# Kernel tuning notes

Hardware: AMD Instinct MI355X
Metric: run time of the kernel (lower is better)

## Reference

```python
import jax, jax.numpy as jnp
import numpy as np

N = 50000      # nodes
E = 800000     # directed edges (avg degree 16)
IN, HID, OUT = 256, 128, 16


def setup_inputs() -> dict:
    key = jax.random.key(0)
    ks = jax.random.split(key, 8)
    x = jax.random.normal(ks[0], (N, IN), dtype=jnp.float32)
    edge_index = jax.random.randint(ks[1], (2, E), 0, N)
    W1 = jax.random.normal(ks[2], (IN, HID), dtype=jnp.float32) * (1.0 / np.sqrt(IN))
    b1 = jnp.zeros((HID,), jnp.float32)
    W2 = jax.random.normal(ks[3], (HID, HID), dtype=jnp.float32) * (1.0 / np.sqrt(HID))
    b2 = jnp.zeros((HID,), jnp.float32)
    Wc = jax.random.normal(ks[4], (HID, OUT), dtype=jnp.float32) * (1.0 / np.sqrt(HID))
    bc = jnp.zeros((OUT,), jnp.float32)
    return {"x": x, "W1": W1, "b1": b1, "W2": W2, "b2": b2,
            "Wc": Wc, "bc": bc, "edge_index": edge_index, "conv_time": 30}


def _gcn_norm(edge_index, n, dtype):
    # add self-loops, compute symmetric GCN normalization D^{-1/2}(A+I)D^{-1/2}
    loops = jnp.arange(n)
    src = jnp.concatenate([edge_index[0], loops])
    dst = jnp.concatenate([edge_index[1], loops])
    deg = jax.ops.segment_sum(jnp.ones_like(dst, dtype=dtype), dst, num_segments=n)
    dinv = jnp.where(deg > 0, jax.lax.rsqrt(deg), jnp.zeros_like(deg))
    norm = dinv[src] * dinv[dst]          # [E+N] edge weights
    return src, dst, norm


def _propagate(h, src, dst, norm, n, hops):
    # hops is a static Python int (conv_time)
    for _ in range(hops):
        h = jax.ops.segment_sum(h[src] * norm[:, None], dst, num_segments=n)
    return h


def reference(x, W1, b1, W2, b2, Wc, bc, edge_index, conv_time):
    n = x.shape[0]
    src, dst, norm = _gcn_norm(edge_index, n, x.dtype)
    # conv1: linear only (conv_time = 0)
    h = jax.nn.relu(x @ W1 + b1)
    # dropout is identity in eval mode
    # conv2: linear + conv_time hops of normalized propagation
    h = _propagate(h @ W2 + b2, src, dst, norm, n, int(conv_time))
    h = jax.nn.relu(h)
    # cls: linear + 1 hop
    h = _propagate(h @ Wc + bc, src, dst, norm, n, 1)
    return h
```

## Files before the change

kernel.cpp:

```cpp
#include <hip/hip_runtime.h>
#include <hip/hip_fp16.h>

#define NNODES 50000
#define NEDGES 800000
#define IN_F   256
#define HID_F  128
#define OUT_F  16
#define HOPS   30

typedef unsigned int u32;

union U32H2 { u32 u; __half2 h; };

__device__ inline float2 upk(u32 v) {
    U32H2 t; t.u = v;
    return __half22float2(t.h);
}
__device__ inline u32 pk2(float a, float b) {
    U32H2 t; t.h = __floats2half2_rn(a, b);
    return t.u;
}


__global__ void k_init_deg(int* __restrict__ deg, int n) {
    int i = blockIdx.x * blockDim.x + threadIdx.x;
    if (i < n) deg[i] = 1;
}

__global__ void k_count(const int* __restrict__ dst, int* __restrict__ deg, int e) {
    int i = blockIdx.x * blockDim.x + threadIdx.x;
    if (i < e) atomicAdd(&deg[dst[i]], 1);
}

__global__ void k_dinv(const int* __restrict__ deg, float* __restrict__ dinv, int n) {
    int i = blockIdx.x * blockDim.x + threadIdx.x;
    if (i < n) dinv[i] = rsqrtf((float)deg[i]);
}

__global__ void k_scan1(const int* __restrict__ deg, int* __restrict__ bsums, int n) {
    __shared__ int sh[256];
    int tid = threadIdx.x;
    int i = blockIdx.x * 256 + tid;
    sh[tid] = (i < n) ? deg[i] : 0;
    __syncthreads();
    for (int ofs = 128; ofs > 0; ofs >>= 1) {
        if (tid < ofs) sh[tid] += sh[tid + ofs];
        __syncthreads();
    }
    if (tid == 0) bsums[blockIdx.x] = sh[0];
}

__global__ void k_scan2(int* __restrict__ bsums, int nb, int* __restrict__ rp, int n) {
    if (threadIdx.x == 0 && blockIdx.x == 0) {
        int run = 0;
        for (int b = 0; b < nb; ++b) { int t = bsums[b]; bsums[b] = run; run += t; }
        rp[n] = run;
    }
}

__global__ void k_scan3(const int* __restrict__ deg, const int* __restrict__ bsums,
                        int* __restrict__ rp, int* __restrict__ cursor, int n) {
    __shared__ int sh[256];
    int tid = threadIdx.x;
    int i = blockIdx.x * 256 + tid;
    int v = (i < n) ? deg[i] : 0;
    sh[tid] = v;
    __syncthreads();
    for (int ofs = 1; ofs < 256; ofs <<= 1) {
        int t = 0;
        if (tid >= ofs) t = sh[tid - ofs];
        __syncthreads();
        sh[tid] += t;
        __syncthreads();
    }
    if (i < n) {
        int excl = sh[tid] - v + bsums[blockIdx.x];
        rp[i] = excl;
        cursor[i] = excl;
    }
}

__global__ void k_scatter(const int* __restrict__ src, const int* __restrict__ dst,
                          const float* __restrict__ dinv, int* __restrict__ cursor,
                          int2* __restrict__ ew, int e, int n) {
    int t = blockIdx.x * blockDim.x + threadIdx.x;
    if (t < e) {
        int s = src[t], d = dst[t];
        int pos = atomicAdd(&cursor[d], 1);
        ew[pos] = make_int2(s, __float_as_int(dinv[s] * dinv[d]));
    } else if (t < e + n) {
        int i = t - e;
        int pos = atomicAdd(&cursor[i], 1);
        float di = dinv[i];
        ew[pos] = make_int2(i, __float_as_int(di * di));
    }
}


template<int K, bool RELU, bool HALF_OUT>
__global__ void k_gemm32(const float* __restrict__ A, const float* __restrict__ W,
                         const float* __restrict__ b, void* __restrict__ C, int M) {
    __shared__ float sa[32][K];
    int tid  = threadIdx.x;
    int row0 = blockIdx.x * 32;
    constexpr int KV = K / 4;

    const float4* A4 = reinterpret_cast<const float4*>(A);
    for (int idx = tid; idx < 32 * KV; idx += 256) {
        int r  = idx / KV;
        int c4 = idx % KV;
        int gr = row0 + r;
        float4 v = (gr < M) ? A4[(size_t)gr * KV + c4]
                            : make_float4(0.f, 0.f, 0.f, 0.f);
        *reinterpret_cast<float4*>(&sa[r][c4 * 4]) = v;
    }
    __syncthreads();

    int tc = tid & 31;
    int tr = tid >> 5;
    float4 acc[4];
#pragma unroll
    for (int j = 0; j < 4; ++j) acc[j] = make_float4(0.f, 0.f, 0.f, 0.f);

    const float4* W4 = reinterpret_cast<const float4*>(W);
    for (int k4 = 0; k4 < KV; ++k4) {
        float4 a[4];
#pragma unroll
        for (int j = 0; j < 4; ++j)
            a[j] = *reinterpret_cast<const float4*>(&sa[tr * 4 + j][k4 * 4]);
        const float* af = reinterpret_cast<const float*>(a);
#pragma unroll
        for (int kk = 0; kk < 4; ++kk) {
            float4 wv = W4[(size_t)(k4 * 4 + kk) * 32 + tc];
#pragma unroll
            for (int j = 0; j < 4; ++j) {
                float av = af[j * 4 + kk];
                acc[j].x += av * wv.x; acc[j].y += av * wv.y;
                acc[j].z += av * wv.z; acc[j].w += av * wv.w;
            }
        }
    }

    float4 bb = reinterpret_cast<const float4*>(b)[tc];
#pragma unroll
    for (int j = 0; j < 4; ++j) {
        int r = row0 + tr * 4 + j;
        if (r < M) {
            float4 v;
            v.x = acc[j].x + bb.x; v.y = acc[j].y + bb.y;
            v.z = acc[j].z + bb.z; v.w = acc[j].w + bb.w;
            if (RELU) {
                v.x = fmaxf(v.x, 0.f); v.y = fmaxf(v.y, 0.f);
                v.z = fmaxf(v.z, 0.f); v.w = fmaxf(v.w, 0.f);
            }
            if (HALF_OUT) {
                u32 lo = pk2(v.x, v.y), hi = pk2(v.z, v.w);
                reinterpret_cast<uint2*>(C)[(size_t)r * 32 + tc] = make_uint2(lo, hi);
            } else {
                reinterpret_cast<float4*>(C)[(size_t)r * 32 + tc] = v;
            }
        }
    }
}


template<bool RELU>
__global__ void k_proph(const u32* __restrict__ Hin, u32* __restrict__ Hout,
                        const int* __restrict__ rp, const int2* __restrict__ ew,
                        int n) {
    int grp  = threadIdx.x >> 3;
    int lane = threadIdx.x & 7;
    int node = blockIdx.x * 32 + grp;
    if (node >= n) return;
    int beg = rp[node], end = rp[node + 1];
    const uint4* H4 = reinterpret_cast<const uint4*>(Hin);

    float acc[16];
#pragma unroll
    for (int i = 0; i < 16; ++i) acc[i] = 0.f;

    auto body = [&](int e) {
        int2 p   = ew[e];
        float ww = __int_as_float(p.y);
        size_t base = (size_t)p.x * 16 + lane * 2;
        uint4 v0 = H4[base];
        uint4 v1 = H4[base + 1];
        const u32* vv = reinterpret_cast<const u32*>(&v0);
#pragma unroll
        for (int q = 0; q < 4; ++q) {
            float2 f = upk(vv[q]);
            acc[q * 2 + 0] += ww * f.x;
            acc[q * 2 + 1] += ww * f.y;
        }
        const u32* vw = reinterpret_cast<const u32*>(&v1);
#pragma unroll
        for (int q = 0; q < 4; ++q) {
            float2 f = upk(vw[q]);
            acc[8 + q * 2 + 0] += ww * f.x;
            acc[8 + q * 2 + 1] += ww * f.y;
        }
    };

    int e = beg;
    for (; e + 1 < end; e += 2) { body(e); body(e + 1); }
    if (e < end) body(e);

    if (RELU) {
#pragma unroll
        for (int i = 0; i < 16; ++i) acc[i] = fmaxf(acc[i], 0.f);
    }
    uint4 o0, o1;
    u32* ov = reinterpret_cast<u32*>(&o0);
#pragma unroll
    for (int q = 0; q < 4; ++q) ov[q] = pk2(acc[q * 2], acc[q * 2 + 1]);
    u32* ow = reinterpret_cast<u32*>(&o1);
#pragma unroll
    for (int q = 0; q < 4; ++q) ow[q] = pk2(acc[8 + q * 2], acc[8 + q * 2 + 1]);
    size_t obase = (size_t)node * 16 + lane * 2;
    reinterpret_cast<uint4*>(Hout)[obase]     = o0;
    reinterpret_cast<uint4*>(Hout)[obase + 1] = o1;
}


__global__ void k_cls_h(const u32* __restrict__ Ah, const float* __restrict__ Wc,
                        const float* __restrict__ bc, float* __restrict__ G, int M) {
    __shared__ float sa[64][132];
    __shared__ float4 sw4[512];
    int tid  = threadIdx.x;
    int row0 = blockIdx.x * 64;

    for (int idx = tid; idx < 512; idx += 256)
        sw4[idx] = reinterpret_cast<const float4*>(Wc)[idx];

    const uint4* A4 = reinterpret_cast<const uint4*>(Ah);
    for (int idx = tid; idx < 64 * 16; idx += 256) {
        int r = idx >> 4, c = idx & 15;
        int gr = row0 + r;
        uint4 v = (gr < M) ? A4[(size_t)gr * 16 + c]
                           : make_uint4(0u, 0u, 0u, 0u);
        float* dst = &sa[r][c * 8];
        const u32* vv = reinterpret_cast<const u32*>(&v);
#pragma unroll
        for (int q = 0; q < 4; ++q) {
            float2 f = upk(vv[q]);
            dst[q * 2 + 0] = f.x;
            dst[q * 2 + 1] = f.y;
        }
    }
    __syncthreads();

    int tc = tid & 3;
    int tr = tid >> 2;
    float4 acc = make_float4(0.f, 0.f, 0.f, 0.f);
    for (int k4 = 0; k4 < 32; ++k4) {
        float4 a = *reinterpret_cast<const float4*>(&sa[tr][k4 * 4]);
        const float* af = reinterpret_cast<const float*>(&a);
#pragma unroll
        for (int kk = 0; kk < 4; ++kk) {
            float4 wv = sw4[(k4 * 4 + kk) * 4 + tc];
            float av = af[kk];
            acc.x += av * wv.x; acc.y += av * wv.y;
            acc.z += av * wv.z; acc.w += av * wv.w;
        }
    }
    int r = row0 + tr;
    if (r < M) {
        float4 bb = reinterpret_cast<const float4*>(bc)[tc];
        acc.x += bb.x; acc.y += bb.y; acc.z += bb.z; acc.w += bb.w;
        reinterpret_cast<float4*>(G)[(size_t)r * 4 + tc] = acc;
    }
}


__global__ void k_prop16(const float* __restrict__ Gin, float* __restrict__ Out,
                         const int* __restrict__ rp, const int2* __restrict__ ew,
                         int n) {
    int g    = blockIdx.x * 64 + (threadIdx.x >> 2);
    int lane = threadIdx.x & 3;
    if (g >= n) return;
    int beg = rp[g], end = rp[g + 1];
    const float4* G4 = reinterpret_cast<const float4*>(Gin);
    float ax = 0.f, ay = 0.f, az = 0.f, aw = 0.f;
    for (int e = beg; e < end; ++e) {
        int2 p   = ew[e];
        float ww = __int_as_float(p.y);
        float4 hv = G4[(size_t)p.x * 4 + lane];
        ax += ww * hv.x; ay += ww * hv.y; az += ww * hv.z; aw += ww * hv.w;
    }
    reinterpret_cast<float4*>(Out)[(size_t)g * 4 + lane] = make_float4(ax, ay, az, aw);
}


extern "C" void kernel_launch(void* const* d_in, const int* in_sizes, int n_in,
                              void* d_out, int out_size, void* d_ws, size_t ws_size,
                              hipStream_t stream) {
    const float* x  = (const float*)d_in[0];
    const float* W1 = (const float*)d_in[1];
    const float* b1 = (const float*)d_in[2];
    const float* W2 = (const float*)d_in[3];
    const float* b2 = (const float*)d_in[4];
    const float* Wc = (const float*)d_in[5];
    const float* bc = (const float*)d_in[6];
    const int*   ei = (const int*)d_in[7];
    const int* srcp = ei;
    const int* dstp = ei + NEDGES;
    float* out = (float*)d_out;

    char* p = (char*)d_ws;
    auto alloc = [&](size_t bytes) -> char* {
        char* r = p;
        p += (bytes + 255) & ~(size_t)255;
        return r;
    };
    int*   deg    = (int*)  alloc(NNODES * 4);
    float* dinv   = (float*)alloc(NNODES * 4);
    int*   rp     = (int*)  alloc((NNODES + 1) * 4);
    int*   cursor = (int*)  alloc(NNODES * 4);
    int*   bsums  = (int*)  alloc(256 * 4);
    int2*  ew     = (int2*) alloc((size_t)(NEDGES + NNODES) * 8);
    float* H0     = (float*)alloc((size_t)NNODES * HID_F * 4);
    u32*   Hh0    = (u32*)  alloc((size_t)NNODES * HID_F * 2);
    u32*   Hh1    = (u32*)  alloc((size_t)NNODES * HID_F * 2);
    float* G      = (float*)alloc((size_t)NNODES * OUT_F * 4);

    const int T = 256;
    auto nb = [](int n, int t) { return (n + t - 1) / t; };

    k_init_deg<<<nb(NNODES, T), T, 0, stream>>>(deg, NNODES);
    k_count<<<nb(NEDGES, T), T, 0, stream>>>(dstp, deg, NEDGES);
    k_dinv<<<nb(NNODES, T), T, 0, stream>>>(deg, dinv, NNODES);
    int NB = nb(NNODES, 256);
    k_scan1<<<NB, 256, 0, stream>>>(deg, bsums, NNODES);
    k_scan2<<<1, 1, 0, stream>>>(bsums, NB, rp, NNODES);
    k_scan3<<<NB, 256, 0, stream>>>(deg, bsums, rp, cursor, NNODES);
    k_scatter<<<nb(NEDGES + NNODES, T), T, 0, stream>>>(srcp, dstp, dinv, cursor,
                                                        ew, NEDGES, NNODES);

    int GB = nb(NNODES, 32);
    k_gemm32<IN_F,  true,  false><<<GB, 256, 0, stream>>>(x,  W1, b1, H0,  NNODES);
    k_gemm32<HID_F, false, true ><<<GB, 256, 0, stream>>>(H0, W2, b2, Hh0, NNODES);

    u32* cur = Hh0;
    u32* nxt = Hh1;
    int PB = nb(NNODES, 32);
    for (int i = 0; i < HOPS; ++i) {
        if (i == HOPS - 1)
            k_proph<true ><<<PB, 256, 0, stream>>>(cur, nxt, rp, ew, NNODES);
        else
            k_proph<false><<<PB, 256, 0, stream>>>(cur, nxt, rp, ew, NNODES);
        u32* t = cur; cur = nxt; nxt = t;
    }

    k_cls_h<<<nb(NNODES, 64), 256, 0, stream>>>(cur, Wc, bc, G, NNODES);
    k_prop16<<<nb(NNODES, 64), 256, 0, stream>>>(G, out, rp, ew, NNODES);
}
```

Before: 1.238 ms.

## Split propagation feature dimension across four blocks per node tile

The propagation kernel now splits each node's 128 half features into four 32-feature chunks, each handled by a separate block. A node gets 4 lanes per chunk, each loading one 16-byte vector per edge. Edge records are read with nontemporal 64-bit loads and outputs are written with nontemporal stores. The aim is more parallelism and lower register pressure. The cost is that every chunk block re-reads the edge list (4x edge-index traffic), and the feature gathers become narrower. An unroll pragma is also added to the GEMM k-loop.

```diff
diff --git a/kernel.cpp b/kernel.cpp
--- a/kernel.cpp
+++ b/kernel.cpp
@@ -9,6 +9,8 @@
 #define HOPS   30
 
 typedef unsigned int u32;
+typedef u32 u32x4 __attribute__((ext_vector_type(4)));
+typedef unsigned long long u64;
 
 union U32H2 { u32 u; __half2 h; };
 
@@ -123,6 +125,7 @@
     for (int j = 0; j < 4; ++j) acc[j] = make_float4(0.f, 0.f, 0.f, 0.f);
 
     const float4* W4 = reinterpret_cast<const float4*>(W);
+#pragma unroll 2
     for (int k4 = 0; k4 < KV; ++k4) {
         float4 a[4];
 #pragma unroll
@@ -165,39 +168,34 @@
 
 
 template<bool RELU>
-__global__ void k_proph(const u32* __restrict__ Hin, u32* __restrict__ Hout,
-                        const int* __restrict__ rp, const int2* __restrict__ ew,
-                        int n) {
-    int grp  = threadIdx.x >> 3;
-    int lane = threadIdx.x & 7;
-    int node = blockIdx.x * 32 + grp;
+__global__ void k_proph4(const u32* __restrict__ Hin, u32* __restrict__ Hout,
+                         const int* __restrict__ rp, const int2* __restrict__ ew,
+                         int n) {
+    int chunk = blockIdx.x & 3;
+    int tile  = blockIdx.x >> 2;
+    int grp   = threadIdx.x >> 2;
+    int lane  = threadIdx.x & 3;
+    int node  = tile * 64 + grp;
     if (node >= n) return;
     int beg = rp[node], end = rp[node + 1];
-    const uint4* H4 = reinterpret_cast<const uint4*>(Hin);
-
-    float acc[16];
-#pragma unroll
-    for (int i = 0; i < 16; ++i) acc[i] = 0.f;
+    const u32x4* H4 = reinterpret_cast<const u32x4*>(Hin);
+    const u64* ew8  = reinterpret_cast<const u64*>(ew);
+    int off = chunk * 4 + lane;
+
+    float acc[8];
+#pragma unroll
+    for (int i = 0; i < 8; ++i) acc[i] = 0.f;
 
     auto body = [&](int e) {
-        int2 p   = ew[e];
-        float ww = __int_as_float(p.y);
-        size_t base = (size_t)p.x * 16 + lane * 2;
-        uint4 v0 = H4[base];
-        uint4 v1 = H4[base + 1];
-        const u32* vv = reinterpret_cast<const u32*>(&v0);
+        u64 pw   = __builtin_nontemporal_load(ew8 + e);
+        int s    = (int)(u32)pw;
+        float ww = __int_as_float((u32)(pw >> 32));
+        u32x4 v  = H4[(size_t)s * 16 + off];
 #pragma unroll
         for (int q = 0; q < 4; ++q) {
-            float2 f = upk(vv[q]);
+            float2 f = upk(v[q]);
             acc[q * 2 + 0] += ww * f.x;
             acc[q * 2 + 1] += ww * f.y;
-        }
-        const u32* vw = reinterpret_cast<const u32*>(&v1);
-#pragma unroll
-        for (int q = 0; q < 4; ++q) {
-            float2 f = upk(vw[q]);
-            acc[8 + q * 2 + 0] += ww * f.x;
-            acc[8 + q * 2 + 1] += ww * f.y;
         }
     };
 
@@ -207,18 +205,13 @@
 
     if (RELU) {
 #pragma unroll
-        for (int i = 0; i < 16; ++i) acc[i] = fmaxf(acc[i], 0.f);
-    }
-    uint4 o0, o1;
-    u32* ov = reinterpret_cast<u32*>(&o0);
-#pragma unroll
-    for (int q = 0; q < 4; ++q) ov[q] = pk2(acc[q * 2], acc[q * 2 + 1]);
-    u32* ow = reinterpret_cast<u32*>(&o1);
-#pragma unroll
-    for (int q = 0; q < 4; ++q) ow[q] = pk2(acc[8 + q * 2], acc[8 + q * 2 + 1]);
-    size_t obase = (size_t)node * 16 + lane * 2;
-    reinterpret_cast<uint4*>(Hout)[obase]     = o0;
-    reinterpret_cast<uint4*>(Hout)[obase + 1] = o1;
+        for (int i = 0; i < 8; ++i) acc[i] = fmaxf(acc[i], 0.f);
+    }
+    u32x4 o;
+#pragma unroll
+    for (int q = 0; q < 4; ++q) o[q] = pk2(acc[q * 2], acc[q * 2 + 1]);
+    __builtin_nontemporal_store(o, reinterpret_cast<u32x4*>(Hout) +
+                                       ((size_t)node * 16 + off));
 }
 
 
@@ -342,12 +335,12 @@
 
     u32* cur = Hh0;
     u32* nxt = Hh1;
-    int PB = nb(NNODES, 32);
+    int PB = nb(NNODES, 64) * 4;
     for (int i = 0; i < HOPS; ++i) {
         if (i == HOPS - 1)
-            k_proph<true ><<<PB, 256, 0, stream>>>(cur, nxt, rp, ew, NNODES);
+            k_proph4<true ><<<PB, 256, 0, stream>>>(cur, nxt, rp, ew, NNODES);
         else
-            k_proph<false><<<PB, 256, 0, stream>>>(cur, nxt, rp, ew, NNODES);
+            k_proph4<false><<<PB, 256, 0, stream>>>(cur, nxt, rp, ew, NNODES);
         u32* t = cur; cur = nxt; nxt = t;
     }
 
```

New measurement: 2.554 ms. 2.06x slower.
